# Performance work log

Hardware: AMD Instinct MI355X
Metric: run time of the kernel (lower is better)

Reference implementation:

```python
import jax, jax.numpy as jnp
import numpy as np

V, E, HID, D = 10000, 512, 512, 14
FEAT = 512  # attention feature dim (== C)


def setup_inputs() -> dict:
    key = jax.random.key(0)
    ks = jax.random.split(key, 20)
    s = 0.02
    inp = {
        "features": jax.random.normal(ks[0], (32, 512, 7, 7), jnp.float32),
        "captions": jax.random.randint(ks[1], (32, 60), 0, V),
        "disease": jax.random.uniform(ks[2], (32, D), jnp.float32),
        # embedding
        "emb": jax.random.normal(ks[3], (V, E), jnp.float32) * s,
        # attention: attn Linear(feat+hid -> hid), v Linear(hid -> 1)
        "W_attn": jax.random.normal(ks[4], (FEAT + HID, HID), jnp.float32) * s,
        "b_attn": jnp.zeros((HID,), jnp.float32),
        "W_v": jax.random.normal(ks[5], (HID, 1), jnp.float32) * s,
        "b_v": jnp.zeros((1,), jnp.float32),
        # attention disease_proj: 14->128->512
        "W_dp1": jax.random.normal(ks[6], (D, 128), jnp.float32) * s,
        "b_dp1": jnp.zeros((128,), jnp.float32),
        "W_dp2": jax.random.normal(ks[7], (128, HID), jnp.float32) * s,
        "b_dp2": jnp.zeros((HID,), jnp.float32),
        # disease_encoder: 14->128->256 (dropout = identity at eval)
        "W_de1": jax.random.normal(ks[8], (D, 128), jnp.float32) * s,
        "b_de1": jnp.zeros((128,), jnp.float32),
        "W_de2": jax.random.normal(ks[9], (128, 256), jnp.float32) * s,
        "b_de2": jnp.zeros((256,), jnp.float32),
        # LSTM (input = E + 512 + 256 = 1280), gate order i,f,g,o
        "W_ih": jax.random.normal(ks[10], (E + FEAT + 256, 4 * HID), jnp.float32) * s,
        "W_hh": jax.random.normal(ks[11], (HID, 4 * HID), jnp.float32) * s,
        "b_ih": jnp.zeros((4 * HID,), jnp.float32),
        "b_hh": jnp.zeros((4 * HID,), jnp.float32),
        # fc: hid -> vocab
        "W_fc": jax.random.normal(ks[12], (HID, V), jnp.float32) * s,
        "b_fc": jnp.zeros((V,), jnp.float32),
    }
    return inp


def reference(features, captions, disease, emb, W_attn, b_attn, W_v, b_v,
              W_dp1, b_dp1, W_dp2, b_dp2, W_de1, b_de1, W_de2, b_de2,
              W_ih, W_hh, b_ih, b_hh, W_fc, b_fc):
    B, C = features.shape[0], features.shape[1]
    f = features.reshape(B, C, -1).transpose(0, 2, 1)  # [B, N, 512]

    embs = emb[captions]  # [B, T, E]

    # time-invariant disease contexts
    dis_ctx = jax.nn.relu(disease @ W_de1 + b_de1) @ W_de2 + b_de2   # [B,256]
    dis_att = jax.nn.relu(disease @ W_dp1 + b_dp1) @ W_dp2 + b_dp2  # [B,HID]

    # split attn weight: energy = tanh(f@Wf + (h+dis_att)@Wh + b)
    Wf, Wh = W_attn[:FEAT], W_attn[FEAT:]
    f_proj = jnp.einsum('bnf,fh->bnh', f, Wf)  # precompute feature part

    def step(carry, emb_t):
        h, c = carry  # [B,HID] each
        hid = h + dis_att
        energy = jnp.tanh(f_proj + (hid @ Wh + b_attn)[:, None, :])  # [B,N,HID]
        scores = (energy @ W_v).squeeze(-1) + b_v[0]                 # [B,N]
        alpha = jax.nn.softmax(scores, axis=1)
        context = jnp.einsum('bn,bnf->bf', alpha, f)                 # [B,512]
        x = jnp.concatenate([emb_t, context, dis_ctx], axis=1)       # [B,1280]
        gates = x @ W_ih + h @ W_hh + b_ih + b_hh
        i, fg, g, o = jnp.split(gates, 4, axis=1)
        c_new = jax.nn.sigmoid(fg) * c + jax.nn.sigmoid(i) * jnp.tanh(g)
        h_new = jax.nn.sigmoid(o) * jnp.tanh(c_new)
        return (h_new, c_new), h_new

    h0 = jnp.zeros((B, HID), f.dtype)
    c0 = jnp.zeros((B, HID), f.dtype)
    _, h_seq = jax.lax.scan(step, (h0, c0), embs.transpose(1, 0, 2))  # [T,B,HID]

    logits = h_seq @ W_fc + b_fc          # [T,B,V]
    return logits.transpose(1, 0, 2)      # [B,T,V]
```

## Files before the change

### kernel.cpp

```cpp
#include <hip/hip_runtime.h>
#include <math.h>

#define BB 32
#define NP 49
#define FE 512
#define HI 512
#define EM 512
#define TT 60
#define G4 2048
#define NV 10000
#define ND 14
#define NBLK 80

typedef __attribute__((ext_vector_type(8))) short short8v;
typedef __attribute__((ext_vector_type(4))) float float4v;

__device__ __forceinline__ float fsig(float x){ return 1.0f/(1.0f+__expf(-x)); }
__device__ __forceinline__ float ftanh(float x){
    x = fminf(fmaxf(x, -15.0f), 15.0f);
    float e = __expf(2.0f*x);
    return (e-1.0f)/(e+1.0f);
}
__device__ __forceinline__ ushort f2bf(float x){
    union { float f; unsigned u; } v; v.f = x;
    unsigned r = v.u + 0x7fff + ((v.u >> 16) & 1);
    return (ushort)(r >> 16);
}
__device__ __forceinline__ float bf2f(ushort h){
    union { float f; unsigned u; } v; v.u = ((unsigned)h) << 16;
    return v.f;
}
__device__ __forceinline__ ushort f2bf_trunc(float x){
    return (ushort)(__float_as_uint(x) >> 16);
}

__global__ void k_transpose(const float* __restrict__ feat, float* __restrict__ fT){
    int b = blockIdx.y;
    int cb = blockIdx.x * 64;
    __shared__ float tile[64][NP+1];
    const float* src = feat + (size_t)b*FE*NP;
    for (int idx = threadIdx.x; idx < 64*NP; idx += 256){
        int cl = idx / NP, n = idx % NP;
        tile[cl][n] = src[(size_t)(cb+cl)*NP + n];
    }
    __syncthreads();
    float* dst = fT + (size_t)b*NP*FE;
    for (int idx = threadIdx.x; idx < 64*NP; idx += 256){
        int cl = idx % 64, n = idx / 64;
        dst[(size_t)n*FE + cb + cl] = tile[cl][n];
    }
}

__global__ void k_disease(const float* __restrict__ dis,
                          const float* __restrict__ Wdp1, const float* __restrict__ bdp1,
                          const float* __restrict__ Wdp2, const float* __restrict__ bdp2,
                          const float* __restrict__ Wde1, const float* __restrict__ bde1,
                          const float* __restrict__ Wde2, const float* __restrict__ bde2,
                          const float* __restrict__ Wattn, const float* __restrict__ battn,
                          const float* __restrict__ Wih, const float* __restrict__ bih,
                          const float* __restrict__ bhh,
                          float* __restrict__ daw, float* __restrict__ disWih){
    int b = blockIdx.x;
    int tid = threadIdx.x;
    __shared__ float d[ND];
    __shared__ float hp[128], he[128];
    __shared__ float datt[HI];
    __shared__ float dctx[256];
    if (tid < ND) d[tid] = dis[b*ND + tid];
    __syncthreads();
    if (tid < 128){
        float accP = bdp1[tid], accE = bde1[tid];
        for (int k=0;k<ND;k++){ accP += d[k]*Wdp1[k*128+tid]; accE += d[k]*Wde1[k*128+tid]; }
        hp[tid] = fmaxf(accP, 0.f);
        he[tid] = fmaxf(accE, 0.f);
    }
    __syncthreads();
    for (int j = tid; j < HI; j += 256){
        float a = bdp2[j];
        for (int k=0;k<128;k++) a += hp[k]*Wdp2[k*HI+j];
        datt[j] = a;
    }
    if (tid < 256){
        float a = bde2[tid];
        for (int k=0;k<128;k++) a += he[k]*Wde2[k*256+tid];
        dctx[tid] = a;
    }
    __syncthreads();
    for (int j = tid; j < HI; j += 256){
        float a = battn[j];
        for (int k=0;k<HI;k++) a += datt[k]*Wattn[(size_t)(FE+k)*HI + j];
        daw[b*HI + j] = a;
    }
    for (int j = tid; j < G4; j += 256){
        float a = bih[j] + bhh[j];
        for (int k=0;k<256;k++) a += dctx[k]*Wih[(size_t)(EM+FE+k)*G4 + j];
        disWih[b*G4 + j] = a;
    }
}

__global__ void k_fproj(const float* __restrict__ fT, const float* __restrict__ Wattn,
                        float* __restrict__ f_proj){
    int b = blockIdx.y, ng = blockIdx.x;
    int n0 = ng*7;
    __shared__ float fr[7][FE];
    const float* src = fT + ((size_t)b*NP + n0)*FE;
    for (int idx = threadIdx.x; idx < 7*FE; idx += 256)
        fr[idx/FE][idx%FE] = src[idx];
    __syncthreads();
    int j0 = threadIdx.x;
    float acc[7][2];
    #pragma unroll
    for (int n=0;n<7;n++){ acc[n][0]=0.f; acc[n][1]=0.f; }
    for (int k=0;k<FE;k++){
        float w0 = Wattn[(size_t)k*HI + j0];
        float w1 = Wattn[(size_t)k*HI + j0 + 256];
        #pragma unroll
        for (int n=0;n<7;n++){
            float fv = fr[n][k];
            acc[n][0] += fv*w0;
            acc[n][1] += fv*w1;
        }
    }
    float* dst = f_proj + ((size_t)b*NP + n0)*HI;
    #pragma unroll
    for (int n=0;n<7;n++){
        dst[(size_t)n*HI + j0] = acc[n][0];
        dst[(size_t)n*HI + j0+256] = acc[n][1];
    }
}

__global__ void k_fwc(const float* __restrict__ fT, const float* __restrict__ Wih,
                      float* __restrict__ fWcP){
    int b = blockIdx.z, ng = blockIdx.y, half = blockIdx.x;
    int n0 = ng*7;
    __shared__ float fr[7][FE];
    const float* src = fT + ((size_t)b*NP + n0)*FE;
    for (int idx = threadIdx.x; idx < 7*FE; idx += 256)
        fr[idx/FE][idx%FE] = src[idx];
    __syncthreads();
    int j0 = half*1024 + threadIdx.x;
    float acc[7][4];
    #pragma unroll
    for (int n=0;n<7;n++){ acc[n][0]=0.f; acc[n][1]=0.f; acc[n][2]=0.f; acc[n][3]=0.f; }
    const float* W = Wih + (size_t)512*G4;
    for (int k=0;k<FE;k++){
        float w0=W[(size_t)k*G4+j0], w1=W[(size_t)k*G4+j0+256], w2=W[(size_t)k*G4+j0+512], w3=W[(size_t)k*G4+j0+768];
        #pragma unroll
        for (int n=0;n<7;n++){
            float fv = fr[n][k];
            acc[n][0]+=fv*w0; acc[n][1]+=fv*w1; acc[n][2]+=fv*w2; acc[n][3]+=fv*w3;
        }
    }
    for (int n=0;n<7;n++){
        #pragma unroll
        for (int q=0;q<4;q++){
            int gc = j0 + q*256;
            int blk = (gc & 511) >> 3, m = gc & 7, g = gc >> 9;
            fWcP[(((size_t)blk*BB + b)*NP + n0+n)*32 + m*4+g] = acc[n][q];
        }
    }
}

__global__ void k_preg(const int* __restrict__ caps, const float* __restrict__ emb,
                       const float* __restrict__ Wih, const float* __restrict__ disWih,
                       float* __restrict__ preGP){
    int rg = blockIdx.y;
    int jt = blockIdx.x;
    int r0 = rg*16;
    __shared__ float er[16][EM];
    __shared__ int bidx[16];
    if (threadIdx.x < 16) bidx[threadIdx.x] = caps[r0 + threadIdx.x];
    __syncthreads();
    for (int idx = threadIdx.x; idx < 16*EM; idx += 256){
        int rl = idx >> 9, k = idx & 511;
        er[rl][k] = emb[(size_t)bidx[rl]*EM + k];
    }
    __syncthreads();
    int j = jt*512 + threadIdx.x;
    float acc[16][2];
    #pragma unroll
    for (int r=0;r<16;r++){ acc[r][0]=0.f; acc[r][1]=0.f; }
    for (int k=0;k<EM;k+=2){
        float w00 = Wih[(size_t)k*G4 + j],     w10 = Wih[(size_t)k*G4 + j + 256];
        float w01 = Wih[(size_t)(k+1)*G4 + j], w11 = Wih[(size_t)(k+1)*G4 + j + 256];
        #pragma unroll
        for (int r=0;r<16;r++){
            float2 e = *(const float2*)&er[r][k];
            acc[r][0] += e.x*w00 + e.y*w01;
            acc[r][1] += e.x*w10 + e.y*w11;
        }
    }
    for (int r=0;r<16;r++){
        int row = r0 + r;
        int b = row/60, t = row - b*60;
        #pragma unroll
        for (int q=0;q<2;q++){
            int gc = j + q*256;
            float v = acc[r][q] + disWih[b*G4 + gc];
            int blk = (gc & 511) >> 3, m = gc & 7, g = gc >> 9;
            preGP[(((size_t)blk*TT + t)*BB + b)*32 + m*4+g] = v;
        }
    }
}

__device__ __forceinline__ void gridbar(int* bar, int tgt){
    __syncthreads();
    if (threadIdx.x == 0)
        __hip_atomic_store(bar + blockIdx.x, tgt, __ATOMIC_RELEASE, __HIP_MEMORY_SCOPE_AGENT);
    if (blockIdx.x == 0 && threadIdx.x < 64){
        int l = threadIdx.x;
        for (;;){
            int v0 = __hip_atomic_load(bar + l, __ATOMIC_RELAXED, __HIP_MEMORY_SCOPE_AGENT);
            int v1 = (l < NBLK-64) ? __hip_atomic_load(bar + 64 + l, __ATOMIC_RELAXED, __HIP_MEMORY_SCOPE_AGENT) : tgt;
            if (__all(v0 >= tgt && v1 >= tgt)) break;
            __builtin_amdgcn_s_sleep(1);
        }
        if (l == 0)
            __hip_atomic_store(bar + 128, tgt, __ATOMIC_RELEASE, __HIP_MEMORY_SCOPE_AGENT);
    }
    if (threadIdx.x == 0){
        while (__hip_atomic_load(bar + 128, __ATOMIC_RELAXED, __HIP_MEMORY_SCOPE_AGENT) < tgt)
            __builtin_amdgcn_s_sleep(1);
    }
    __syncthreads();
}

__launch_bounds__(512, 1)
__global__ void k_scan_coop(const float* __restrict__ f_proj, const float* __restrict__ fWcP,
                            const float* __restrict__ preGP, const float* __restrict__ daw,
                            const float* __restrict__ Wattn, const float* __restrict__ Whh,
                            const float* __restrict__ Wv,
                            float* __restrict__ h_seq, float* __restrict__ a_buf,
                            float* __restrict__ scores, int* __restrict__ bar){
    __shared__ __align__(16) ushort h_hi[16384], h_lo[16384];
    __shared__ __align__(16) ushort w_hi[16384], w_lo[16384];
    __shared__ float al[32*52];
    __shared__ float gbuf[32*33];
    __shared__ float daw_lds[32*32];
    __shared__ float gv[32*36];
    __shared__ float cst[256];
    __shared__ float wvl[512];
    int bk = blockIdx.x;
    int tid = threadIdx.x;
    int lane = tid & 63, wave = tid >> 6;
    bool isGate = bk < 64;

    {
        int k = tid;
        if (isGate){
            const float* wr = Whh + (size_t)k*G4 + bk*8;
            #pragma unroll
            for (int g = 0; g < 4; g++){
                float4 v0 = *(const float4*)(wr + g*512);
                float4 v1 = *(const float4*)(wr + g*512 + 4);
                float vv[8] = {v0.x,v0.y,v0.z,v0.w,v1.x,v1.y,v1.z,v1.w};
                #pragma unroll
                for (int u = 0; u < 8; u++){
                    int c = u*4 + g;
                    ushort hi = f2bf(vv[u]);
                    ushort lo = f2bf(vv[u] - bf2f(hi));
                    int idx = (c*512 + k) ^ ((c&7)<<3);
                    w_hi[idx] = hi; w_lo[idx] = lo;
                }
            }
        } else {
            const float* wr = Wattn + (size_t)(FE + k)*HI + (bk-64)*32;
            #pragma unroll
            for (int cq = 0; cq < 8; cq++){
                float4 v = *(const float4*)(wr + cq*4);
                float vv[4] = {v.x,v.y,v.z,v.w};
                #pragma unroll
                for (int q = 0; q < 4; q++){
                    int c = cq*4 + q;
                    ushort hi = f2bf(vv[q]);
                    ushort lo = f2bf(vv[q] - bf2f(hi));
                    int idx = (c*512 + k) ^ ((c&7)<<3);
                    w_hi[idx] = hi; w_lo[idx] = lo;
                }
            }
            for (int i = tid; i < 1024; i += 512){
                int b = i >> 5, c = i & 31;
                daw_lds[i] = daw[b*HI + (bk-64)*32 + c];
            }
        }
        if (tid < 256) cst[tid] = 0.f;
        wvl[tid] = Wv[tid];
    }
    __syncthreads();

    int tgt = 0;
    for (int t = 0; t < TT; t++){
        if (t == 0){
            uint4 z = make_uint4(0,0,0,0);
            #pragma unroll
            for (int it = 0; it < 4; it++){
                int flat = (it*512 + tid)*8;
                int b = flat >> 9, k = flat & 511;
                int di = (b*512 + k) ^ ((b&7)<<3);
                *(uint4*)&h_hi[di] = z;
                *(uint4*)&h_lo[di] = z;
            }
        } else {
            const float* hs = h_seq + (size_t)(t-1)*BB*HI;
            #pragma unroll
            for (int it = 0; it < 4; it++){
                int flat = (it*512 + tid)*8;
                int b = flat >> 9, k = flat & 511;
                float4 v0 = *(const float4*)(hs + flat);
                float4 v1 = *(const float4*)(hs + flat + 4);
                float fv[8] = {v0.x,v0.y,v0.z,v0.w,v1.x,v1.y,v1.z,v1.w};
                union { ushort u[8]; uint4 v; } ph, pl;
                #pragma unroll
                for (int j = 0; j < 8; j++){
                    ushort hi = f2bf(fv[j]);
                    ph.u[j] = hi;
                    pl.u[j] = f2bf(fv[j] - bf2f(hi));
                }
                int di = (b*512 + k) ^ ((b&7)<<3);
                *(uint4*)&h_hi[di] = ph.v;
                *(uint4*)&h_lo[di] = pl.v;
            }
        }
        __syncthreads();

        if (wave < 4){
            int rbase = (wave >> 1) * 16, cbase = (wave & 1) * 16;
            int m = lane & 15, kg = lane >> 4;
            int arow = rbase + m, bcol = cbase + m;
            int abase = arow*512 + kg*8, axr = (arow&7)<<3;
            int bbase = bcol*512 + kg*8, bxr = (bcol&7)<<3;
            float4v acc = {0.f,0.f,0.f,0.f};
            #pragma unroll
            for (int ks = 0; ks < 16; ks++){
                int ai = (abase + ks*32) ^ axr;
                int bi = (bbase + ks*32) ^ bxr;
                short8v ahi = *(const short8v*)&h_hi[ai];
                short8v alo = *(const short8v*)&h_lo[ai];
                short8v bhi = *(const short8v*)&w_hi[bi];
                short8v blo = *(const short8v*)&w_lo[bi];
                acc = __builtin_amdgcn_mfma_f32_16x16x32_bf16(ahi, bhi, acc, 0,0,0);
                acc = __builtin_amdgcn_mfma_f32_16x16x32_bf16(alo, bhi, acc, 0,0,0);
                acc = __builtin_amdgcn_mfma_f32_16x16x32_bf16(ahi, blo, acc, 0,0,0);
            }
            int ccol = cbase + (lane & 15);
            int crow0 = rbase + (lane >> 4)*4;
            if (isGate){
                #pragma unroll
                for (int r = 0; r < 4; r++)
                    gbuf[(crow0+r)*33 + ccol] = acc[r];
            } else {
                int cb = (bk-64)*32;
                float* ab = a_buf + (size_t)t*BB*HI;
                #pragma unroll
                for (int r = 0; r < 4; r++)
                    ab[(size_t)(crow0+r)*HI + cb + ccol] = acc[r] + daw_lds[(crow0+r)*32 + ccol];
            }
        }
        gridbar(bar, ++tgt);

        {
            int wid = tid >> 6, l = tid & 63;
            for (int p = bk + wid*NBLK; p < BB*NP; p += NBLK*8){
                int pb = p / NP, pn = p - pb*NP;
                const float* fpn = f_proj + ((size_t)pb*NP + pn)*HI;
                const float* at  = a_buf + ((size_t)t*BB + pb)*HI;
                int j = l*8;
                float4 f0 = *(const float4*)(fpn + j);
                float4 a0 = *(const float4*)(at + j);
                float4 f1 = *(const float4*)(fpn + j + 4);
                float4 a1 = *(const float4*)(at + j + 4);
                float s = wvl[j+0]*ftanh(f0.x + a0.x)
                        + wvl[j+1]*ftanh(f0.y + a0.y)
                        + wvl[j+2]*ftanh(f0.z + a0.z)
                        + wvl[j+3]*ftanh(f0.w + a0.w)
                        + wvl[j+4]*ftanh(f1.x + a1.x)
                        + wvl[j+5]*ftanh(f1.y + a1.y)
                        + wvl[j+6]*ftanh(f1.z + a1.z)
                        + wvl[j+7]*ftanh(f1.w + a1.w);
                #pragma unroll
                for (int off = 32; off; off >>= 1) s += __shfl_xor(s, off);
                if (l == 0) scores[t*(BB*NP) + p] = s;
            }
        }
        gridbar(bar, ++tgt);

        if (isGate){
            int hw = tid >> 5, l32 = tid & 31;
            #pragma unroll
            for (int rep = 0; rep < 2; rep++){
                int b = hw + rep*16;
                const float* sb = scores + t*(BB*NP) + b*NP;
                float s0 = sb[l32];
                float s1 = (l32 < 17) ? sb[32 + l32] : -1e30f;
                float m = fmaxf(s0, s1);
                #pragma unroll
                for (int off = 16; off; off >>= 1) m = fmaxf(m, __shfl_xor(m, off, 32));
                float e0 = __expf(s0 - m);
                float e1 = (l32 < 17) ? __expf(s1 - m) : 0.f;
                float sm = e0 + e1;
                #pragma unroll
                for (int off = 16; off; off >>= 1) sm += __shfl_xor(sm, off, 32);
                float inv = 1.f / sm;
                al[b*52 + l32] = e0*inv;
                if (l32 < 17) al[b*52 + 32 + l32] = e1*inv;
            }
            __syncthreads();
            {
                int b = tid >> 4, cp = tid & 15;
                float g0 = gbuf[b*33 + cp];
                float g1 = gbuf[b*33 + cp + 16];
                const float* pgp = preGP + (((size_t)bk*TT + t)*BB + b)*32;
                g0 += pgp[cp];
                g1 += pgp[cp + 16];
                const float* fw = fWcP + (((size_t)bk*BB + b)*NP)*32;
                for (int n = 0; n < NP; n++){
                    float av = al[b*52 + n];
                    g0 += av*fw[n*32 + cp];
                    g1 += av*fw[n*32 + cp + 16];
                }
                gv[b*36 + cp]      = g0;
                gv[b*36 + cp + 16] = g1;
            }
            __syncthreads();
            if (tid < 256){
                int b = tid >> 3, m = tid & 7;
                float gi = gv[b*36 + m*4 + 0];
                float gf = gv[b*36 + m*4 + 1];
                float gg = gv[b*36 + m*4 + 2];
                float go = gv[b*36 + m*4 + 3];
                float cn = fsig(gf)*cst[b*8 + m] + fsig(gi)*ftanh(gg);
                float hn = fsig(go)*ftanh(cn);
                cst[b*8 + m] = cn;
                h_seq[(size_t)t*BB*HI + b*HI + bk*8 + m] = hn;
            }
        }
        gridbar(bar, ++tgt);
    }
}

__launch_bounds__(512, 1)
__global__ void k_logits(const float* __restrict__ h_seq, const float* __restrict__ Wfc,
                         const float* __restrict__ bfc, float* __restrict__ out){
    __shared__ __align__(16) ushort h_hi[16384], h_lo[16384];
    int t = blockIdx.x, vt = blockIdx.y;
    int tid = threadIdx.x, lane = tid & 63, wave = tid >> 6;
    const float* hs = h_seq + (size_t)t*BB*HI;
    #pragma unroll
    for (int it = 0; it < 4; it++){
        int flat = (it*512 + tid)*8;
        int b = flat >> 9, k = flat & 511;
        float4 v0 = *(const float4*)(hs + flat);
        float4 v1 = *(const float4*)(hs + flat + 4);
        float fv[8] = {v0.x,v0.y,v0.z,v0.w,v1.x,v1.y,v1.z,v1.w};
        union { ushort u[8]; uint4 v; } ph, pl;
        #pragma unroll
        for (int j = 0; j < 8; j++){
            ushort hi = f2bf(fv[j]);
            ph.u[j] = hi;
            pl.u[j] = f2bf(fv[j] - bf2f(hi));
        }
        int di = (b*512 + k) ^ ((b&7)<<3);
        *(uint4*)&h_hi[di] = ph.v;
        *(uint4*)&h_lo[di] = pl.v;
    }
    __syncthreads();

    int m = lane & 15, kg = lane >> 4;
    int cb = vt*256 + wave*32;
    int a0 = m*512 + kg*8;
    int a1 = (16+m)*512 + kg*8;
    int axr = (m&7)<<3;
    float4v acc[2][2];
    acc[0][0]=(float4v){0,0,0,0}; acc[0][1]=(float4v){0,0,0,0};
    acc[1][0]=(float4v){0,0,0,0}; acc[1][1]=(float4v){0,0,0,0};
    const short8v bz = {0,0,0,0,0,0,0,0};

    for (int ks = 0; ks < 16; ks++){
        short8v ah0 = *(const short8v*)&h_hi[(a0 + ks*32) ^ axr];
        short8v al0 = *(const short8v*)&h_lo[(a0 + ks*32) ^ axr];
        short8v ah1 = *(const short8v*)&h_hi[(a1 + ks*32) ^ axr];
        short8v al1 = *(const short8v*)&h_lo[(a1 + ks*32) ^ axr];
        #pragma unroll
        for (int cj = 0; cj < 2; cj++){
            int v = cb + cj*16 + m;
            short8v bhi = bz, blo = bz;
            if (v < NV){
                int k0 = ks*32 + kg*8;
                const float* wp = Wfc + (size_t)k0*NV + v;
                float w[8];
                #pragma unroll
                for (int i = 0; i < 8; i++) w[i] = wp[(size_t)i*NV];
                union { ushort u[8]; short8v s; } bh, bl;
                #pragma unroll
                for (int i = 0; i < 8; i++){
                    ushort hi = f2bf(w[i]);
                    bh.u[i] = hi;
                    bl.u[i] = f2bf_trunc(w[i] - bf2f(hi));
                }
                bhi = bh.s; blo = bl.s;
            }
            acc[0][cj] = __builtin_amdgcn_mfma_f32_16x16x32_bf16(ah0, bhi, acc[0][cj], 0,0,0);
            acc[0][cj] = __builtin_amdgcn_mfma_f32_16x16x32_bf16(al0, bhi, acc[0][cj], 0,0,0);
            acc[0][cj] = __builtin_amdgcn_mfma_f32_16x16x32_bf16(ah0, blo, acc[0][cj], 0,0,0);
            acc[1][cj] = __builtin_amdgcn_mfma_f32_16x16x32_bf16(ah1, bhi, acc[1][cj], 0,0,0);
            acc[1][cj] = __builtin_amdgcn_mfma_f32_16x16x32_bf16(al1, bhi, acc[1][cj], 0,0,0);
            acc[1][cj] = __builtin_amdgcn_mfma_f32_16x16x32_bf16(ah1, blo, acc[1][cj], 0,0,0);
        }
    }
    #pragma unroll
    for (int cj = 0; cj < 2; cj++){
        int v = cb + cj*16 + m;
        if (v < NV){
            float bias = bfc[v];
            #pragma unroll
            for (int ri = 0; ri < 2; ri++){
                int b0 = ri*16 + kg*4;
                #pragma unroll
                for (int r = 0; r < 4; r++)
                    out[((size_t)(b0+r)*TT + t)*NV + v] = acc[ri][cj][r] + bias;
            }
        }
    }
}

extern "C" void kernel_launch(void* const* d_in, const int* in_sizes, int n_in,
                              void* d_out, int out_size, void* d_ws, size_t ws_size,
                              hipStream_t stream){
    const float* features = (const float*)d_in[0];
    const int*   captions = (const int*)d_in[1];
    const float* disease  = (const float*)d_in[2];
    const float* emb      = (const float*)d_in[3];
    const float* W_attn   = (const float*)d_in[4];
    const float* b_attn   = (const float*)d_in[5];
    const float* W_v      = (const float*)d_in[6];
    const float* W_dp1    = (const float*)d_in[8];
    const float* b_dp1    = (const float*)d_in[9];
    const float* W_dp2    = (const float*)d_in[10];
    const float* b_dp2    = (const float*)d_in[11];
    const float* W_de1    = (const float*)d_in[12];
    const float* b_de1    = (const float*)d_in[13];
    const float* W_de2    = (const float*)d_in[14];
    const float* b_de2    = (const float*)d_in[15];
    const float* W_ih     = (const float*)d_in[16];
    const float* W_hh     = (const float*)d_in[17];
    const float* b_ih     = (const float*)d_in[18];
    const float* b_hh     = (const float*)d_in[19];
    const float* W_fc     = (const float*)d_in[20];
    const float* b_fc     = (const float*)d_in[21];
    float* out = (float*)d_out;

    const size_t N_HSEQ = (size_t)TT*BB*HI;
    float* h_seq = (float*)d_ws;
    int*   bar   = (int*)((char*)d_ws + N_HSEQ*sizeof(float));

    const size_t N_FT   = (size_t)BB*NP*FE;
    const size_t N_FP   = (size_t)BB*NP*HI;
    const size_t N_FWC  = (size_t)BB*NP*G4;
    const size_t N_PREG = (size_t)BB*TT*G4;
    const size_t N_ABUF = (size_t)TT*BB*HI;
    const size_t N_SC   = (size_t)TT*BB*NP;
    float* fT     = out;
    float* f_proj = fT + N_FT;
    float* fWcP   = f_proj + N_FP;
    float* preGP  = fWcP + N_FWC;
    float* a_buf  = preGP + N_PREG;
    float* scores = a_buf + N_ABUF;
    float* disWih = scores + N_SC;
    float* daw    = disWih + (size_t)BB*G4;

    hipMemsetAsync(bar, 0, 1024, stream);
    k_transpose<<<dim3(8,BB),256,0,stream>>>(features, fT);
    k_disease<<<BB,256,0,stream>>>(disease, W_dp1,b_dp1,W_dp2,b_dp2,
                                   W_de1,b_de1,W_de2,b_de2,
                                   W_attn,b_attn, W_ih,b_ih,b_hh,
                                   daw, disWih);
    k_fproj<<<dim3(7,BB),256,0,stream>>>(fT, W_attn, f_proj);
    k_fwc<<<dim3(2,7,BB),256,0,stream>>>(fT, W_ih, fWcP);
    k_preg<<<dim3(4,120),256,0,stream>>>(captions, emb, W_ih, disWih, preGP);
    k_scan_coop<<<NBLK,512,0,stream>>>(f_proj, fWcP, preGP, daw,
                                       W_attn, W_hh, W_v,
                                       h_seq, a_buf, scores, bar);
    k_logits<<<dim3(TT,40),512,0,stream>>>(h_seq, W_fc, b_fc, out);
}
```

Measured before the change: 1.835 ms.

## Move precompute GEMMs to split-bf16 MFMA tiles with shared staging helper

The three precompute GEMMs (feature projection, feature-to-gate, embedding-to-gate) change from scalar FP32 FMA loops to 32-row tiles computed with bf16 MFMA. Each operand is split into hi/lo bf16 parts and three products are summed to approximate FP32 accuracy. Staging and the MFMA inner loop are factored into shared helpers that the logits kernel also uses, and the grids are re-tiled to 512-thread blocks. The lo part is now rounded by truncation instead of round-to-nearest, which can shift numerics slightly. These kernels are a small share of total time next to the sequential scan.

```diff
diff --git a/kernel.cpp b/kernel.cpp
--- a/kernel.cpp
+++ b/kernel.cpp
@@ -98,107 +98,157 @@
     }
 }
 
+__device__ __forceinline__ void stage_rows32(const float* __restrict__ src0, size_t ldsrc,
+                                             const int* __restrict__ rowmap,
+                                             ushort* h_hi, ushort* h_lo, int tid){
+    #pragma unroll
+    for (int it = 0; it < 4; it++){
+        int flat = (it*512 + tid)*8;
+        int row = flat >> 9, k = flat & 511;
+        const float* src = src0 + (rowmap ? (size_t)rowmap[row]*ldsrc : (size_t)row*ldsrc) + k;
+        float4 v0 = *(const float4*)(src);
+        float4 v1 = *(const float4*)(src + 4);
+        float fv[8] = {v0.x,v0.y,v0.z,v0.w,v1.x,v1.y,v1.z,v1.w};
+        union { ushort u[8]; uint4 v; } ph, pl;
+        #pragma unroll
+        for (int j = 0; j < 8; j++){
+            ushort hi = f2bf(fv[j]);
+            ph.u[j] = hi;
+            pl.u[j] = f2bf_trunc(fv[j] - bf2f(hi));
+        }
+        int di = (row*512 + k) ^ ((row&7)<<3);
+        *(uint4*)&h_hi[di] = ph.v;
+        *(uint4*)&h_lo[di] = pl.v;
+    }
+}
+
+__device__ __forceinline__ void mfma_32x32(const ushort* h_hi, const ushort* h_lo,
+                                           const float* __restrict__ Wb, size_t ldB, int col0,
+                                           int lane, float4v acc[2][2]){
+    int m = lane & 15, kg = lane >> 4;
+    int a0 = m*512 + kg*8;
+    int a1 = (16+m)*512 + kg*8;
+    int axr = (m&7)<<3;
+    for (int ks = 0; ks < 16; ks++){
+        short8v ah0 = *(const short8v*)&h_hi[(a0 + ks*32) ^ axr];
+        short8v al0 = *(const short8v*)&h_lo[(a0 + ks*32) ^ axr];
+        short8v ah1 = *(const short8v*)&h_hi[(a1 + ks*32) ^ axr];
+        short8v al1 = *(const short8v*)&h_lo[(a1 + ks*32) ^ axr];
+        #pragma unroll
+        for (int cj = 0; cj < 2; cj++){
+            int v = col0 + cj*16 + m;
+            int k0 = ks*32 + kg*8;
+            const float* wp = Wb + (size_t)k0*ldB + v;
+            float w[8];
+            #pragma unroll
+            for (int i = 0; i < 8; i++) w[i] = wp[(size_t)i*ldB];
+            union { ushort u[8]; short8v s; } bh, bl;
+            #pragma unroll
+            for (int i = 0; i < 8; i++){
+                ushort hi = f2bf(w[i]);
+                bh.u[i] = hi;
+                bl.u[i] = f2bf_trunc(w[i] - bf2f(hi));
+            }
+            acc[0][cj] = __builtin_amdgcn_mfma_f32_16x16x32_bf16(ah0, bh.s, acc[0][cj], 0,0,0);
+            acc[0][cj] = __builtin_amdgcn_mfma_f32_16x16x32_bf16(al0, bh.s, acc[0][cj], 0,0,0);
+            acc[0][cj] = __builtin_amdgcn_mfma_f32_16x16x32_bf16(ah0, bl.s, acc[0][cj], 0,0,0);
+            acc[1][cj] = __builtin_amdgcn_mfma_f32_16x16x32_bf16(ah1, bh.s, acc[1][cj], 0,0,0);
+            acc[1][cj] = __builtin_amdgcn_mfma_f32_16x16x32_bf16(al1, bh.s, acc[1][cj], 0,0,0);
+            acc[1][cj] = __builtin_amdgcn_mfma_f32_16x16x32_bf16(ah1, bl.s, acc[1][cj], 0,0,0);
+        }
+    }
+}
+
+__launch_bounds__(512, 1)
 __global__ void k_fproj(const float* __restrict__ fT, const float* __restrict__ Wattn,
                         float* __restrict__ f_proj){
-    int b = blockIdx.y, ng = blockIdx.x;
-    int n0 = ng*7;
-    __shared__ float fr[7][FE];
-    const float* src = fT + ((size_t)b*NP + n0)*FE;
-    for (int idx = threadIdx.x; idx < 7*FE; idx += 256)
-        fr[idx/FE][idx%FE] = src[idx];
-    __syncthreads();
-    int j0 = threadIdx.x;
-    float acc[7][2];
+    __shared__ __align__(16) ushort h_hi[16384], h_lo[16384];
+    int r0 = blockIdx.x*32, vt = blockIdx.y;
+    int tid = threadIdx.x, lane = tid & 63, wave = tid >> 6;
+    stage_rows32(fT + (size_t)r0*FE, FE, nullptr, h_hi, h_lo, tid);
+    __syncthreads();
+    int col0 = vt*256 + wave*32;
+    float4v acc[2][2];
+    acc[0][0]=(float4v){0,0,0,0}; acc[0][1]=(float4v){0,0,0,0};
+    acc[1][0]=(float4v){0,0,0,0}; acc[1][1]=(float4v){0,0,0,0};
+    mfma_32x32(h_hi, h_lo, Wattn, HI, col0, lane, acc);
+    int m = lane & 15, kg = lane >> 4;
     #pragma unroll
-    for (int n=0;n<7;n++){ acc[n][0]=0.f; acc[n][1]=0.f; }
-    for (int k=0;k<FE;k++){
-        float w0 = Wattn[(size_t)k*HI + j0];
-        float w1 = Wattn[(size_t)k*HI + j0 + 256];
+    for (int cj = 0; cj < 2; cj++){
+        int col = col0 + cj*16 + m;
         #pragma unroll
-        for (int n=0;n<7;n++){
-            float fv = fr[n][k];
-            acc[n][0] += fv*w0;
-            acc[n][1] += fv*w1;
-        }
-    }
-    float* dst = f_proj + ((size_t)b*NP + n0)*HI;
-    #pragma unroll
-    for (int n=0;n<7;n++){
-        dst[(size_t)n*HI + j0] = acc[n][0];
-        dst[(size_t)n*HI + j0+256] = acc[n][1];
-    }
-}
-
+        for (int ri = 0; ri < 2; ri++){
+            int arow0 = ri*16 + kg*4;
+            #pragma unroll
+            for (int r = 0; r < 4; r++)
+                f_proj[(size_t)(r0 + arow0 + r)*HI + col] = acc[ri][cj][r];
+        }
+    }
+}
+
+__launch_bounds__(512, 1)
 __global__ void k_fwc(const float* __restrict__ fT, const float* __restrict__ Wih,
                       float* __restrict__ fWcP){
-    int b = blockIdx.z, ng = blockIdx.y, half = blockIdx.x;
-    int n0 = ng*7;
-    __shared__ float fr[7][FE];
-    const float* src = fT + ((size_t)b*NP + n0)*FE;
-    for (int idx = threadIdx.x; idx < 7*FE; idx += 256)
-        fr[idx/FE][idx%FE] = src[idx];
-    __syncthreads();
-    int j0 = half*1024 + threadIdx.x;
-    float acc[7][4];
+    __shared__ __align__(16) ushort h_hi[16384], h_lo[16384];
+    int r0 = blockIdx.x*32, vt = blockIdx.y;
+    int tid = threadIdx.x, lane = tid & 63, wave = tid >> 6;
+    stage_rows32(fT + (size_t)r0*FE, FE, nullptr, h_hi, h_lo, tid);
+    __syncthreads();
+    int col0 = vt*256 + wave*32;
+    float4v acc[2][2];
+    acc[0][0]=(float4v){0,0,0,0}; acc[0][1]=(float4v){0,0,0,0};
+    acc[1][0]=(float4v){0,0,0,0}; acc[1][1]=(float4v){0,0,0,0};
+    mfma_32x32(h_hi, h_lo, Wih + (size_t)FE*G4, G4, col0, lane, acc);
+    int m = lane & 15, kg = lane >> 4;
     #pragma unroll
-    for (int n=0;n<7;n++){ acc[n][0]=0.f; acc[n][1]=0.f; acc[n][2]=0.f; acc[n][3]=0.f; }
-    const float* W = Wih + (size_t)512*G4;
-    for (int k=0;k<FE;k++){
-        float w0=W[(size_t)k*G4+j0], w1=W[(size_t)k*G4+j0+256], w2=W[(size_t)k*G4+j0+512], w3=W[(size_t)k*G4+j0+768];
+    for (int cj = 0; cj < 2; cj++){
+        int gc = col0 + cj*16 + m;
+        int blk = (gc & 511) >> 3, m8 = gc & 7, g = gc >> 9;
         #pragma unroll
-        for (int n=0;n<7;n++){
-            float fv = fr[n][k];
-            acc[n][0]+=fv*w0; acc[n][1]+=fv*w1; acc[n][2]+=fv*w2; acc[n][3]+=fv*w3;
-        }
-    }
-    for (int n=0;n<7;n++){
-        #pragma unroll
-        for (int q=0;q<4;q++){
-            int gc = j0 + q*256;
-            int blk = (gc & 511) >> 3, m = gc & 7, g = gc >> 9;
-            fWcP[(((size_t)blk*BB + b)*NP + n0+n)*32 + m*4+g] = acc[n][q];
-        }
-    }
-}
-
+        for (int ri = 0; ri < 2; ri++){
+            int arow0 = ri*16 + kg*4;
+            #pragma unroll
+            for (int r = 0; r < 4; r++){
+                int R = r0 + arow0 + r;
+                int b = R / 49, n = R - b*49;
+                fWcP[(((size_t)blk*BB + b)*NP + n)*32 + m8*4 + g] = acc[ri][cj][r];
+            }
+        }
+    }
+}
+
+__launch_bounds__(512, 1)
 __global__ void k_preg(const int* __restrict__ caps, const float* __restrict__ emb,
                        const float* __restrict__ Wih, const float* __restrict__ disWih,
                        float* __restrict__ preGP){
-    int rg = blockIdx.y;
-    int jt = blockIdx.x;
-    int r0 = rg*16;
-    __shared__ float er[16][EM];
-    __shared__ int bidx[16];
-    if (threadIdx.x < 16) bidx[threadIdx.x] = caps[r0 + threadIdx.x];
-    __syncthreads();
-    for (int idx = threadIdx.x; idx < 16*EM; idx += 256){
-        int rl = idx >> 9, k = idx & 511;
-        er[rl][k] = emb[(size_t)bidx[rl]*EM + k];
-    }
-    __syncthreads();
-    int j = jt*512 + threadIdx.x;
-    float acc[16][2];
+    __shared__ __align__(16) ushort h_hi[16384], h_lo[16384];
+    __shared__ int bidx[32];
+    int r0 = blockIdx.x*32, vt = blockIdx.y;
+    int tid = threadIdx.x, lane = tid & 63, wave = tid >> 6;
+    if (tid < 32) bidx[tid] = caps[r0 + tid];
+    __syncthreads();
+    stage_rows32(emb, EM, bidx, h_hi, h_lo, tid);
+    __syncthreads();
+    int col0 = vt*256 + wave*32;
+    float4v acc[2][2];
+    acc[0][0]=(float4v){0,0,0,0}; acc[0][1]=(float4v){0,0,0,0};
+    acc[1][0]=(float4v){0,0,0,0}; acc[1][1]=(float4v){0,0,0,0};
+    mfma_32x32(h_hi, h_lo, Wih, G4, col0, lane, acc);
+    int m = lane & 15, kg = lane >> 4;
     #pragma unroll
-    for (int r=0;r<16;r++){ acc[r][0]=0.f; acc[r][1]=0.f; }
-    for (int k=0;k<EM;k+=2){
-        float w00 = Wih[(size_t)k*G4 + j],     w10 = Wih[(size_t)k*G4 + j + 256];
-        float w01 = Wih[(size_t)(k+1)*G4 + j], w11 = Wih[(size_t)(k+1)*G4 + j + 256];
+    for (int cj = 0; cj < 2; cj++){
+        int gc = col0 + cj*16 + m;
+        int blk = (gc & 511) >> 3, m8 = gc & 7, g = gc >> 9;
         #pragma unroll
-        for (int r=0;r<16;r++){
-            float2 e = *(const float2*)&er[r][k];
-            acc[r][0] += e.x*w00 + e.y*w01;
-            acc[r][1] += e.x*w10 + e.y*w11;
-        }
-    }
-    for (int r=0;r<16;r++){
-        int row = r0 + r;
-        int b = row/60, t = row - b*60;
-        #pragma unroll
-        for (int q=0;q<2;q++){
-            int gc = j + q*256;
-            float v = acc[r][q] + disWih[b*G4 + gc];
-            int blk = (gc & 511) >> 3, m = gc & 7, g = gc >> 9;
-            preGP[(((size_t)blk*TT + t)*BB + b)*32 + m*4+g] = v;
+        for (int ri = 0; ri < 2; ri++){
+            int arow0 = ri*16 + kg*4;
+            #pragma unroll
+            for (int r = 0; r < 4; r++){
+                int R = r0 + arow0 + r;
+                int b = R / 60, t = R - b*60;
+                preGP[(((size_t)blk*TT + t)*BB + b)*32 + m8*4 + g] =
+                    acc[ri][cj][r] + disWih[b*G4 + gc];
+            }
         }
     }
 }
@@ -444,25 +494,7 @@
     __shared__ __align__(16) ushort h_hi[16384], h_lo[16384];
     int t = blockIdx.x, vt = blockIdx.y;
     int tid = threadIdx.x, lane = tid & 63, wave = tid >> 6;
-    const float* hs = h_seq + (size_t)t*BB*HI;
-    #pragma unroll
-    for (int it = 0; it < 4; it++){
-        int flat = (it*512 + tid)*8;
-        int b = flat >> 9, k = flat & 511;
-        float4 v0 = *(const float4*)(hs + flat);
-        float4 v1 = *(const float4*)(hs + flat + 4);
-        float fv[8] = {v0.x,v0.y,v0.z,v0.w,v1.x,v1.y,v1.z,v1.w};
-        union { ushort u[8]; uint4 v; } ph, pl;
-        #pragma unroll
-        for (int j = 0; j < 8; j++){
-            ushort hi = f2bf(fv[j]);
-            ph.u[j] = hi;
-            pl.u[j] = f2bf(fv[j] - bf2f(hi));
-        }
-        int di = (b*512 + k) ^ ((b&7)<<3);
-        *(uint4*)&h_hi[di] = ph.v;
-        *(uint4*)&h_lo[di] = pl.v;
-    }
+    stage_rows32(h_seq + (size_t)t*BB*HI, HI, nullptr, h_hi, h_lo, tid);
     __syncthreads();
 
     int m = lane & 15, kg = lane >> 4;
@@ -574,9 +606,9 @@
                                    W_de1,b_de1,W_de2,b_de2,
                                    W_attn,b_attn, W_ih,b_ih,b_hh,
                                    daw, disWih);
-    k_fproj<<<dim3(7,BB),256,0,stream>>>(fT, W_attn, f_proj);
-    k_fwc<<<dim3(2,7,BB),256,0,stream>>>(fT, W_ih, fWcP);
-    k_preg<<<dim3(4,120),256,0,stream>>>(captions, emb, W_ih, disWih, preGP);
+    k_fproj<<<dim3(49,2),512,0,stream>>>(fT, W_attn, f_proj);
+    k_fwc<<<dim3(49,8),512,0,stream>>>(fT, W_ih, fWcP);
+    k_preg<<<dim3(60,8),512,0,stream>>>(captions, emb, W_ih, disWih, preGP);
     k_scan_coop<<<NBLK,512,0,stream>>>(f_proj, fWcP, preGP, daw,
                                        W_attn, W_hh, W_v,
                                        h_seq, a_buf, scores, bar);
```

After: 1.668 ms. 1.1x faster.
